# Performance work log

Measured on AMD Instinct MI355X. Metric: run time of the kernel, lower is better.

## Reference

```python
import jax, jax.numpy as jnp
import numpy as np

B = 1048576
T = 3
HD = [30, 45, 40, 30]  # lstm_hidden_dim
IN = 8


def _w(key, out_d, in_d):
    return jax.random.normal(key, (out_d, in_d), dtype=jnp.float32) * 0.1


def setup_inputs() -> dict:
    key = jax.random.key(0)
    ks = jax.random.split(key, 18)
    return {
        "x": jax.random.normal(ks[0], (B, T, IN), dtype=jnp.float32),
        # hidden_transform: Linear(8+30 -> 30), bias=True (default)
        "ht_W": _w(ks[1], HD[0], IN + HD[0]),
        "ht_b": jax.random.normal(ks[2], (HD[0],), dtype=jnp.float32) * 0.1,
        # LSTMCell.main MLP: 60->30, 30->45, 45->40, 40->30, all bias=True
        "m_W0": _w(ks[3], HD[0], 2 * HD[0]),
        "m_b0": jax.random.normal(ks[4], (HD[0],), dtype=jnp.float32) * 0.1,
        "m_W1": _w(ks[5], HD[1], HD[0]),
        "m_b1": jax.random.normal(ks[6], (HD[1],), dtype=jnp.float32) * 0.1,
        "m_W2": _w(ks[7], HD[2], HD[1]),
        "m_b2": jax.random.normal(ks[8], (HD[2],), dtype=jnp.float32) * 0.1,
        "m_W3": _w(ks[9], HD[3], HD[2]),
        "m_b3": jax.random.normal(ks[10], (HD[3],), dtype=jnp.float32) * 0.1,
        # gate linear: 30 -> 120
        "g_W": _w(ks[11], 4 * HD[3], HD[3]),
        "g_b": jax.random.normal(ks[12], (4 * HD[3],), dtype=jnp.float32) * 0.1,
        # predict heads
        "p1_W": _w(ks[13], 10, HD[3]),
        "p1_b": jax.random.normal(ks[14], (10,), dtype=jnp.float32) * 0.1,
        "p2_W": _w(ks[15], 1, 10),
        "p2_b": jax.random.normal(ks[16], (1,), dtype=jnp.float32) * 0.1,
    }


def reference(x, ht_W, ht_b, m_W0, m_b0, m_W1, m_b1, m_W2, m_b2, m_W3, m_b3,
              g_W, g_b, p1_W, p1_b, p2_W, p2_b):
    b = x.shape[0]
    hidden = jnp.zeros((b, HD[0]), dtype=x.dtype)
    cell = jnp.zeros((b, HD[0]), dtype=x.dtype)
    for t in range(T):  # fixed tiny time loop (time_step=3)
        # hidden_transform(cat([x_t, hidden]))
        hs = jnp.concatenate([x[:, t, :], hidden], axis=1) @ ht_W.T + ht_b
        # NOTE: original passes [hidden_state, cell] as cur_state, so h_cur == hs
        combined = jnp.concatenate([hs, hs], axis=1)  # [B, 60]
        a = jnp.tanh(combined @ m_W0.T + m_b0)
        a = jnp.tanh(a @ m_W1.T + m_b1)
        a = jnp.tanh(a @ m_W2.T + m_b2)
        a = jnp.tanh(a @ m_W3.T + m_b3)
        gates = jnp.tanh(a @ g_W.T + g_b)  # extra tanh BEFORE the split (faithful)
        cc_i, cc_f, cc_o, cc_g = jnp.split(gates, 4, axis=1)
        i_g = jax.nn.sigmoid(cc_i)
        f_g = jax.nn.sigmoid(cc_f)
        o_g = jax.nn.sigmoid(cc_o)
        g_g = jnp.tanh(cc_g)
        cell = f_g * cell + i_g * g_g
        hidden = o_g * jnp.tanh(cell)
    out = hidden @ p1_W.T + p1_b
    out = out @ p2_W.T + p2_b  # [B, 1]
    return out
```

## Files before the change

### kernel.cpp

```cpp
#include <hip/hip_runtime.h>


#define NB 1048576

typedef unsigned short u16t;
typedef __attribute__((ext_vector_type(4))) _Float16 half4;
typedef __attribute__((ext_vector_type(4))) float f32x4;
typedef __attribute__((ext_vector_type(2))) int int2v;

#define MFMA __builtin_amdgcn_mfma_f32_16x16x16f16
#define TSCL 2.8853900817779268f

#define NTILE 47
#define WFSZ (NTILE * 256)
#define BIASOFF (WFSZ / 2)
#define BHS 0
#define BB0 32
#define BB1 64
#define BB2 112
#define BB3 160
#define BGB 192
#define BPW 320
#define BPB 352
#define NBIAS 360

__global__ void prep_kernel(const float* __restrict__ htW, const float* __restrict__ htb,
                            const float* __restrict__ w0,  const float* __restrict__ b0,
                            const float* __restrict__ w1,  const float* __restrict__ b1,
                            const float* __restrict__ w2,  const float* __restrict__ b2,
                            const float* __restrict__ w3,  const float* __restrict__ b3,
                            const float* __restrict__ gw,  const float* __restrict__ gb,
                            const float* __restrict__ p1w, const float* __restrict__ p1b,
                            const float* __restrict__ p2w, const float* __restrict__ p2b,
                            float* __restrict__ ws) {
  int tid = threadIdx.x;
  const signed char msel[NTILE] = {0,0,0,0,0,0, 1,1,1,1, 2,2,2,2,2,2,
                                   3,3,3,3,3,3,3,3,3, 4,4,4,4,4,4,
                                   5,5,5,5,5,5,5,5, 5,5,5,5,5,5,5,5};
  const unsigned char tm0[NTILE] = {0,0,0,16,16,16, 0,0,16,16, 0,0,16,16,32,32,
                                    0,0,0,16,16,16,32,32,32, 0,0,0,16,16,16,
                                    0,0,32,32,64,64,96,96, 16,16,48,48,80,80,112,112};
  const unsigned char tk0[NTILE] = {0,16,32,0,16,32, 0,16,0,16, 0,16,0,16,0,16,
                                    0,16,32,0,16,32,0,16,32, 0,16,32,0,16,32,
                                    0,16,0,16,0,16,0,16, 0,16,0,16,0,16,0,16};
  u16t* wf = (u16t*)ws;
  for (int i = tid; i < WFSZ; i += 256) {
    int tau = i >> 8, s = i & 255, l = s >> 2, ii = s & 3;
    int k = tk0[tau] + ((l >> 4) << 2) + ii;
    float v = 0.f;
    int sel = msel[tau];
    if (sel == 5) {
      int g = tm0[tau] >> 5;
      int j = (tm0[tau] & 16) + (l & 15);
      if (j < 30 && k < 30) v = gw[(g * 30 + j) * 30 + k];
    } else {
      int m = tm0[tau] + (l & 15);
      switch (sel) {
        case 0: if (m < 30 && k < 38) v = htW[m * 38 + k]; break;
        case 1: if (m < 30 && k < 30) v = w0[m * 60 + k] + w0[m * 60 + 30 + k]; break;
        case 2: if (m < 45 && k < 30) v = w1[m * 30 + k]; break;
        case 3: if (m < 40 && k < 45) v = w2[m * 45 + k]; break;
        default: if (m < 30 && k < 40) v = w3[m * 40 + k]; break;
      }
    }
    if (tau >= 6) v *= TSCL;
    _Float16 h = (_Float16)v;
    wf[i] = __builtin_bit_cast(u16t, h);
  }
  float* bias = ws + BIASOFF;
  for (int i = tid; i < NBIAS; i += 256) {
    float v = 0.f;
    if (i < 32)       { if (i < 30) v = htb[i]; }
    else if (i < 64)  { int j = i - 32;  if (j < 30) v = b0[j]; }
    else if (i < 112) { int j = i - 64;  if (j < 45) v = b1[j]; }
    else if (i < 160) { int j = i - 112; if (j < 40) v = b2[j]; }
    else if (i < 192) { int j = i - 160; if (j < 30) v = b3[j]; }
    else if (i < 320) { int j = i - 192; int g = j >> 5, q = j & 31;
                        if (q < 30) v = gb[g * 30 + q]; }
    else if (i < 352) { int j = i - 320;
                        if (j < 30) { float a = 0.f;
                          for (int m = 0; m < 10; m++) a += p2w[m] * p1w[m * 30 + j];
                          v = a; } }
    else if (i == 352){ float a = p2b[0];
                        for (int m = 0; m < 10; m++) a += p2w[m] * p1b[m];
                        v = a; }
    if (i >= 32 && i < 320) v *= TSCL;
    bias[i] = v;
  }
}

__device__ __forceinline__ float etanh(float y) {
  float u = __builtin_amdgcn_exp2f(y);
  return 1.0f - 2.0f * __builtin_amdgcn_rcpf(u + 1.0f);
}
__device__ __forceinline__ float ftanh(float v) {
  float u = __builtin_amdgcn_exp2f(v * TSCL);
  return 1.0f - 2.0f * __builtin_amdgcn_rcpf(u + 1.0f);
}
__device__ __forceinline__ float psig(float t) {
  float t2 = t * t;
  float p = fmaf(t2, fmaf(t2, 0.001734f, -0.020646f), 0.249971f);
  return fmaf(t, p, 0.5f);
}
__device__ __forceinline__ float ptanh(float t) {
  float t2 = t * t;
  float p = fmaf(t2, fmaf(t2, fmaf(t2, -0.022665f, 0.111808f), -0.326967f), 0.999418f);
  return t * p;
}

__device__ __forceinline__ half4 tp4(f32x4 c) {
  half4 r;
#pragma unroll
  for (int i = 0; i < 4; i++) r[i] = (_Float16)etanh(c[i]);
  return r;
}
__device__ __forceinline__ half4 p4(f32x4 c) {
  half4 r;
#pragma unroll
  for (int i = 0; i < 4; i++) r[i] = (_Float16)c[i];
  return r;
}

__global__ void __launch_bounds__(256) lstm_main(const float* __restrict__ x,
                                                 const float* __restrict__ ws,
                                                 float* __restrict__ out) {
  __shared__ __align__(16) u16t wfL[WFSZ];
  __shared__ __align__(16) float biasL[NBIAS];
  int tid = threadIdx.x;
  {
    const float4* src = (const float4*)ws;
    for (int i = tid; i < WFSZ / 8; i += 256) ((float4*)wfL)[i] = src[i];
    for (int i = tid; i < NBIAS / 4; i += 256) ((float4*)biasL)[i] = src[WFSZ / 8 + i];
  }
  __syncthreads();

  int lane = tid & 63, wv = tid >> 6;
  int q = lane >> 4;
  int eb = blockIdx.x * 64 + wv * 16;
  int elem = eb + (lane & 15);

  auto ldW = [&](int tau) -> half4 {
    return __builtin_bit_cast(half4, *(const int2v*)((const char*)wfL + tau * 512 + lane * 8));
  };
  auto ldbias = [&](int boff, int mt) -> f32x4 {
    float4 bv = *(const float4*)&biasL[boff + mt * 16 + q * 4];
    return (f32x4){bv.x, bv.y, bv.z, bv.w};
  };

  half4 h0pk = (half4)0, h1pk = (half4)0;
  float cell0[4] = {0.f, 0.f, 0.f, 0.f}, cell1[4] = {0.f, 0.f, 0.f, 0.f};
  float hid0[4], hid1[4];

  for (int t = 0; t < 3; t++) {
    float4 xv = *(const float4*)(x + (size_t)elem * 24 + t * 8 + (q & 1) * 4);
    half4 hx;
    hx[0] = (_Float16)xv.x; hx[1] = (_Float16)xv.y;
    hx[2] = (_Float16)xv.z; hx[3] = (_Float16)xv.w;
    int2v h0i = __builtin_bit_cast(int2v, h0pk);
    int2v h1i = __builtin_bit_cast(int2v, h1pk);
    int2v sh0 = {__shfl_xor(h0i.x, 32), __shfl_xor(h0i.y, 32)};
    int2v sh1 = {__shfl_xor(h1i.x, 32), __shfl_xor(h1i.y, 32)};
    half4 B0 = (q < 2) ? hx : __builtin_bit_cast(half4, sh0);
    half4 B1 = __builtin_bit_cast(half4, (q < 2) ? sh0 : sh1);
    half4 B2 = __builtin_bit_cast(half4, sh1);

    f32x4 c0 = ldbias(BHS, 0), c1 = ldbias(BHS, 1);
    c0 = MFMA(ldW(0), B0, c0, 0, 0, 0);
    c0 = MFMA(ldW(1), B1, c0, 0, 0, 0);
    c0 = MFMA(ldW(2), B2, c0, 0, 0, 0);
    c1 = MFMA(ldW(3), B0, c1, 0, 0, 0);
    c1 = MFMA(ldW(4), B1, c1, 0, 0, 0);
    c1 = MFMA(ldW(5), B2, c1, 0, 0, 0);
    half4 f0 = p4(c0), f1 = p4(c1);

    c0 = ldbias(BB0, 0); c1 = ldbias(BB0, 1);
    c0 = MFMA(ldW(6), f0, c0, 0, 0, 0);
    c0 = MFMA(ldW(7), f1, c0, 0, 0, 0);
    c1 = MFMA(ldW(8), f0, c1, 0, 0, 0);
    c1 = MFMA(ldW(9), f1, c1, 0, 0, 0);
    half4 g0 = tp4(c0), g1 = tp4(c1);

    f32x4 d0 = ldbias(BB1, 0), d1 = ldbias(BB1, 1), d2 = ldbias(BB1, 2);
    d0 = MFMA(ldW(10), g0, d0, 0, 0, 0);
    d0 = MFMA(ldW(11), g1, d0, 0, 0, 0);
    d1 = MFMA(ldW(12), g0, d1, 0, 0, 0);
    d1 = MFMA(ldW(13), g1, d1, 0, 0, 0);
    d2 = MFMA(ldW(14), g0, d2, 0, 0, 0);
    d2 = MFMA(ldW(15), g1, d2, 0, 0, 0);
    half4 e0 = tp4(d0), e1 = tp4(d1), e2 = tp4(d2);

    f32x4 u0 = ldbias(BB2, 0), u1 = ldbias(BB2, 1), u2 = ldbias(BB2, 2);
    u0 = MFMA(ldW(16), e0, u0, 0, 0, 0);
    u0 = MFMA(ldW(17), e1, u0, 0, 0, 0);
    u0 = MFMA(ldW(18), e2, u0, 0, 0, 0);
    u1 = MFMA(ldW(19), e0, u1, 0, 0, 0);
    u1 = MFMA(ldW(20), e1, u1, 0, 0, 0);
    u1 = MFMA(ldW(21), e2, u1, 0, 0, 0);
    u2 = MFMA(ldW(22), e0, u2, 0, 0, 0);
    u2 = MFMA(ldW(23), e1, u2, 0, 0, 0);
    u2 = MFMA(ldW(24), e2, u2, 0, 0, 0);
    half4 v0 = tp4(u0), v1 = tp4(u1), v2 = tp4(u2);

    c0 = ldbias(BB3, 0); c1 = ldbias(BB3, 1);
    c0 = MFMA(ldW(25), v0, c0, 0, 0, 0);
    c0 = MFMA(ldW(26), v1, c0, 0, 0, 0);
    c0 = MFMA(ldW(27), v2, c0, 0, 0, 0);
    c1 = MFMA(ldW(28), v0, c1, 0, 0, 0);
    c1 = MFMA(ldW(29), v1, c1, 0, 0, 0);
    c1 = MFMA(ldW(30), v2, c1, 0, 0, 0);
    half4 w0f = tp4(c0), w1f = tp4(c1);

    f32x4 ai = ldbias(BGB + 0, 0), af = ldbias(BGB + 32, 0);
    f32x4 ao = ldbias(BGB + 64, 0), ag = ldbias(BGB + 96, 0);
    ai = MFMA(ldW(31), w0f, ai, 0, 0, 0); ai = MFMA(ldW(32), w1f, ai, 0, 0, 0);
    af = MFMA(ldW(33), w0f, af, 0, 0, 0); af = MFMA(ldW(34), w1f, af, 0, 0, 0);
    ao = MFMA(ldW(35), w0f, ao, 0, 0, 0); ao = MFMA(ldW(36), w1f, ao, 0, 0, 0);
    ag = MFMA(ldW(37), w0f, ag, 0, 0, 0); ag = MFMA(ldW(38), w1f, ag, 0, 0, 0);
#pragma unroll
    for (int r = 0; r < 4; r++) {
      float ti = etanh(ai[r]), tf = etanh(af[r]);
      float to = etanh(ao[r]), tg = etanh(ag[r]);
      float ig = psig(ti), fg = psig(tf), og = psig(to);
      float gg = ptanh(tg);
      float c = fmaf(fg, cell0[r], ig * gg);
      cell0[r] = c;
      hid0[r] = og * ftanh(c);
    }
    ai = ldbias(BGB + 0, 1); af = ldbias(BGB + 32, 1);
    ao = ldbias(BGB + 64, 1); ag = ldbias(BGB + 96, 1);
    ai = MFMA(ldW(39), w0f, ai, 0, 0, 0); ai = MFMA(ldW(40), w1f, ai, 0, 0, 0);
    af = MFMA(ldW(41), w0f, af, 0, 0, 0); af = MFMA(ldW(42), w1f, af, 0, 0, 0);
    ao = MFMA(ldW(43), w0f, ao, 0, 0, 0); ao = MFMA(ldW(44), w1f, ao, 0, 0, 0);
    ag = MFMA(ldW(45), w0f, ag, 0, 0, 0); ag = MFMA(ldW(46), w1f, ag, 0, 0, 0);
#pragma unroll
    for (int r = 0; r < 4; r++) {
      float ti = etanh(ai[r]), tf = etanh(af[r]);
      float to = etanh(ao[r]), tg = etanh(ag[r]);
      float ig = psig(ti), fg = psig(tf), og = psig(to);
      float gg = ptanh(tg);
      float c = fmaf(fg, cell1[r], ig * gg);
      cell1[r] = c;
      hid1[r] = og * ftanh(c);
    }
#pragma unroll
    for (int r = 0; r < 4; r++) {
      h0pk[r] = (_Float16)hid0[r];
      h1pk[r] = (_Float16)hid1[r];
    }
  }
  float4 pw0 = *(const float4*)&biasL[BPW + q * 4];
  float4 pw1 = *(const float4*)&biasL[BPW + 16 + q * 4];
  float s = pw0.x * hid0[0] + pw0.y * hid0[1] + pw0.z * hid0[2] + pw0.w * hid0[3]
          + pw1.x * hid1[0] + pw1.y * hid1[1] + pw1.z * hid1[2] + pw1.w * hid1[3];
  s += __shfl_xor(s, 16);
  s += __shfl_xor(s, 32);
  if (lane < 16) out[eb + lane] = biasL[BPB] + s;
}

extern "C" void kernel_launch(void* const* d_in, const int* in_sizes, int n_in,
                              void* d_out, int out_size, void* d_ws, size_t ws_size,
                              hipStream_t stream) {
  const float* x   = (const float*)d_in[0];
  const float* htW = (const float*)d_in[1];
  const float* htb = (const float*)d_in[2];
  const float* w0  = (const float*)d_in[3];
  const float* b0  = (const float*)d_in[4];
  const float* w1  = (const float*)d_in[5];
  const float* b1  = (const float*)d_in[6];
  const float* w2  = (const float*)d_in[7];
  const float* b2  = (const float*)d_in[8];
  const float* w3  = (const float*)d_in[9];
  const float* b3  = (const float*)d_in[10];
  const float* gw  = (const float*)d_in[11];
  const float* gb  = (const float*)d_in[12];
  const float* p1w = (const float*)d_in[13];
  const float* p1b = (const float*)d_in[14];
  const float* p2w = (const float*)d_in[15];
  const float* p2b = (const float*)d_in[16];
  float* ws = (float*)d_ws;
  float* out = (float*)d_out;

  hipLaunchKernelGGL(prep_kernel, dim3(1), dim3(256), 0, stream,
                     htW, htb, w0, b0, w1, b1, w2, b2, w3, b3, gw, gb,
                     p1w, p1b, p2w, p2b, ws);
  hipLaunchKernelGGL(lstm_main, dim3(NB / 64), dim3(256), 0, stream, x, ws, out);
}
```

Before: 307.5 us.

## Batch tanh reciprocals, use packed fp16 conversion, polynomial cell tanh

```diff
diff --git a/kernel.cpp b/kernel.cpp
--- a/kernel.cpp
+++ b/kernel.cpp
@@ -4,6 +4,7 @@
 #define NB 1048576
 
 typedef unsigned short u16t;
+typedef __attribute__((ext_vector_type(2))) __fp16 fp16x2;
 typedef __attribute__((ext_vector_type(4))) _Float16 half4;
 typedef __attribute__((ext_vector_type(4))) float f32x4;
 typedef __attribute__((ext_vector_type(2))) int int2v;
@@ -89,14 +90,35 @@
   }
 }
 
-__device__ __forceinline__ float etanh(float y) {
-  float u = __builtin_amdgcn_exp2f(y);
-  return 1.0f - 2.0f * __builtin_amdgcn_rcpf(u + 1.0f);
-}
-__device__ __forceinline__ float ftanh(float v) {
-  float u = __builtin_amdgcn_exp2f(v * TSCL);
-  return 1.0f - 2.0f * __builtin_amdgcn_rcpf(u + 1.0f);
-}
+__device__ __forceinline__ half4 pk4(float a, float b, float c, float d) {
+  fp16x2 lo = __builtin_amdgcn_cvt_pkrtz(a, b);
+  fp16x2 hi = __builtin_amdgcn_cvt_pkrtz(c, d);
+  int2v r = {__builtin_bit_cast(int, lo), __builtin_bit_cast(int, hi)};
+  return __builtin_bit_cast(half4, r);
+}
+
+__device__ __forceinline__ f32x4 qtanh(f32x4 y) {
+  float u0 = __builtin_amdgcn_exp2f(y[0]);
+  float u1 = __builtin_amdgcn_exp2f(y[1]);
+  float u2 = __builtin_amdgcn_exp2f(y[2]);
+  float u3 = __builtin_amdgcn_exp2f(y[3]);
+  float D0 = u0 + 1.f, D1 = u1 + 1.f, D2 = u2 + 1.f, D3 = u3 + 1.f;
+  float D01 = D0 * D1, D23 = D2 * D3;
+  float v = __builtin_amdgcn_rcpf(D01 * D23);
+  float v01 = v * D23, v23 = v * D01;
+  f32x4 t;
+  t[0] = fmaf(-2.f, v01 * D1, 1.f);
+  t[1] = fmaf(-2.f, v01 * D0, 1.f);
+  t[2] = fmaf(-2.f, v23 * D3, 1.f);
+  t[3] = fmaf(-2.f, v23 * D2, 1.f);
+  return t;
+}
+
+__device__ __forceinline__ half4 tp4(f32x4 c) {
+  f32x4 t = qtanh(c);
+  return pk4(t[0], t[1], t[2], t[3]);
+}
+
 __device__ __forceinline__ float psig(float t) {
   float t2 = t * t;
   float p = fmaf(t2, fmaf(t2, 0.001734f, -0.020646f), 0.249971f);
@@ -107,18 +129,10 @@
   float p = fmaf(t2, fmaf(t2, fmaf(t2, -0.022665f, 0.111808f), -0.326967f), 0.999418f);
   return t * p;
 }
-
-__device__ __forceinline__ half4 tp4(f32x4 c) {
-  half4 r;
-#pragma unroll
-  for (int i = 0; i < 4; i++) r[i] = (_Float16)etanh(c[i]);
-  return r;
-}
-__device__ __forceinline__ half4 p4(f32x4 c) {
-  half4 r;
-#pragma unroll
-  for (int i = 0; i < 4; i++) r[i] = (_Float16)c[i];
-  return r;
+__device__ __forceinline__ float ctanh(float c) {
+  float y = c * c;
+  float p = fmaf(y, fmaf(y, fmaf(y, -0.0194316f, 0.109571f), -0.328327f), 0.999778f);
+  return c * p;
 }
 
 __global__ void __launch_bounds__(256) lstm_main(const float* __restrict__ x,
@@ -153,9 +167,7 @@
 
   for (int t = 0; t < 3; t++) {
     float4 xv = *(const float4*)(x + (size_t)elem * 24 + t * 8 + (q & 1) * 4);
-    half4 hx;
-    hx[0] = (_Float16)xv.x; hx[1] = (_Float16)xv.y;
-    hx[2] = (_Float16)xv.z; hx[3] = (_Float16)xv.w;
+    half4 hx = pk4(xv.x, xv.y, xv.z, xv.w);
     int2v h0i = __builtin_bit_cast(int2v, h0pk);
     int2v h1i = __builtin_bit_cast(int2v, h1pk);
     int2v sh0 = {__shfl_xor(h0i.x, 32), __shfl_xor(h0i.y, 32)};
@@ -171,7 +183,8 @@
     c1 = MFMA(ldW(3), B0, c1, 0, 0, 0);
     c1 = MFMA(ldW(4), B1, c1, 0, 0, 0);
     c1 = MFMA(ldW(5), B2, c1, 0, 0, 0);
-    half4 f0 = p4(c0), f1 = p4(c1);
+    half4 f0 = pk4(c0[0], c0[1], c0[2], c0[3]);
+    half4 f1 = pk4(c1[0], c1[1], c1[2], c1[3]);
 
     c0 = ldbias(BB0, 0); c1 = ldbias(BB0, 1);
     c0 = MFMA(ldW(6), f0, c0, 0, 0, 0);
@@ -218,13 +231,12 @@
     ag = MFMA(ldW(37), w0f, ag, 0, 0, 0); ag = MFMA(ldW(38), w1f, ag, 0, 0, 0);
 #pragma unroll
     for (int r = 0; r < 4; r++) {
-      float ti = etanh(ai[r]), tf = etanh(af[r]);
-      float to = etanh(ao[r]), tg = etanh(ag[r]);
-      float ig = psig(ti), fg = psig(tf), og = psig(to);
-      float gg = ptanh(tg);
+      f32x4 tq = qtanh((f32x4){ai[r], af[r], ao[r], ag[r]});
+      float ig = psig(tq[0]), fg = psig(tq[1]), og = psig(tq[2]);
+      float gg = ptanh(tq[3]);
       float c = fmaf(fg, cell0[r], ig * gg);
       cell0[r] = c;
-      hid0[r] = og * ftanh(c);
+      hid0[r] = og * ctanh(c);
     }
     ai = ldbias(BGB + 0, 1); af = ldbias(BGB + 32, 1);
     ao = ldbias(BGB + 64, 1); ag = ldbias(BGB + 96, 1);
@@ -234,19 +246,15 @@
     ag = MFMA(ldW(45), w0f, ag, 0, 0, 0); ag = MFMA(ldW(46), w1f, ag, 0, 0, 0);
 #pragma unroll
     for (int r = 0; r < 4; r++) {
-      float ti = etanh(ai[r]), tf = etanh(af[r]);
-      float to = etanh(ao[r]), tg = etanh(ag[r]);
-      float ig = psig(ti), fg = psig(tf), og = psig(to);
-      float gg = ptanh(tg);
+      f32x4 tq = qtanh((f32x4){ai[r], af[r], ao[r], ag[r]});
+      float ig = psig(tq[0]), fg = psig(tq[1]), og = psig(tq[2]);
+      float gg = ptanh(tq[3]);
       float c = fmaf(fg, cell1[r], ig * gg);
       cell1[r] = c;
-      hid1[r] = og * ftanh(c);
+      hid1[r] = og * ctanh(c);
     }
-#pragma unroll
-    for (int r = 0; r < 4; r++) {
-      h0pk[r] = (_Float16)hid0[r];
-      h1pk[r] = (_Float16)hid1[r];
-    }
+    h0pk = pk4(hid0[0], hid0[1], hid0[2], hid0[3]);
+    h1pk = pk4(hid1[0], hid1[1], hid1[2], hid1[3]);
   }
   float4 pw0 = *(const float4*)&biasL[BPW + q * 4];
   float4 pw1 = *(const float4*)&biasL[BPW + 16 + q * 4];
```

Measured after the change: 323.7 us. 1.05x slower.
